# Kernel tuning notes

Hardware: AMD Instinct MI355X
Metric: run time of the kernel (lower is better)

The kernel has to match this reference:

```python
import jax, jax.numpy as jnp
import numpy as np
import math

B, T, HID = 2, 2048, 2048
NH, KVH, HD = 16, 4, 128  # num_heads, kv_heads, head_dim


def rotate_half(x):
    x1, x2 = x[..., : x.shape[-1] // 2], x[..., x.shape[-1] // 2 :]
    return jnp.concatenate([-x2, x1], axis=-1)


def setup_inputs() -> dict:
    key = jax.random.key(0)
    ks = jax.random.split(key, 6)
    hidden_states = jax.random.normal(ks[0], (B, T, HID), dtype=jnp.float32)
    # additive causal mask (0 on/below diag, -inf-ish above)
    causal = jnp.triu(jnp.full((T, T), -1e9, dtype=jnp.float32), k=1)
    attention_mask = causal[None, None, :, :]
    # real RoPE angles
    inv_freq = 1.0 / (10000.0 ** (np.arange(0, HD, 2, dtype=np.float32) / HD))
    t = np.arange(T, dtype=np.float32)
    freqs = np.einsum('t,d->td', t, inv_freq)
    emb = np.concatenate([freqs, freqs], axis=-1)  # (T, HD)
    cos = jnp.asarray(np.cos(emb))[None, None, :, :]
    sin = jnp.asarray(np.sin(emb))[None, None, :, :]
    s = 0.02
    Wq = jax.random.normal(ks[1], (HID, NH * HD), dtype=jnp.float32) * s
    Wk = jax.random.normal(ks[2], (HID, KVH * HD), dtype=jnp.float32) * s
    Wv = jax.random.normal(ks[3], (HID, KVH * HD), dtype=jnp.float32) * s
    Wo = jax.random.normal(ks[4], (HID, HID), dtype=jnp.float32) * s
    return dict(hidden_states=hidden_states, attention_mask=attention_mask,
                cos=cos, sin=sin, Wq=Wq, Wk=Wk, Wv=Wv, Wo=Wo)


def reference(hidden_states, attention_mask, cos, sin, Wq, Wk, Wv, Wo):
    b, t, _ = hidden_states.shape
    # projections; weights stored (in, out) so y = x @ W
    q = (hidden_states @ Wq).reshape(b, t, NH, HD).transpose(0, 2, 1, 3)   # (B,H,T,D)
    k = (hidden_states @ Wk).reshape(b, t, KVH, HD).transpose(0, 2, 1, 3)  # (B,Hkv,T,D)
    v = (hidden_states @ Wv).reshape(b, t, KVH, HD).transpose(0, 2, 1, 3)
    # RoPE
    c, s = cos[:, :, :t, :], sin[:, :, :t, :]
    q = q * c + rotate_half(q) * s
    k = k * c + rotate_half(k) * s
    # GQA: repeat_interleave kv heads
    rf = NH // KVH
    k = jnp.repeat(k, rf, axis=1)
    v = jnp.repeat(v, rf, axis=1)
    scores = jnp.einsum('bhtd,bhsd->bhts', q, k) / math.sqrt(HD)
    scores = scores + attention_mask
    probs = jax.nn.softmax(scores.astype(jnp.float32), axis=-1).astype(q.dtype)
    ctx = jnp.einsum('bhts,bhsd->bhtd', probs, v)
    ctx = ctx.transpose(0, 2, 1, 3).reshape(b, t, HID)
    return ctx @ Wo
```

## Files before the change

kernel.cpp:

```cpp
#include <hip/hip_runtime.h>
#include <hip/hip_bf16.h>
#include <math.h>

typedef __bf16 bf16;
typedef __bf16 bf16x4 __attribute__((ext_vector_type(4)));
typedef __bf16 bf16x8 __attribute__((ext_vector_type(8)));
typedef float f32x4 __attribute__((ext_vector_type(4)));

#define B_   2
#define T_   2048
#define HID_ 2048
#define NH_  16
#define KVH_ 4
#define HD_  128

__device__ __forceinline__ void gload_lds16(const bf16* g, bf16* l) {
    __builtin_amdgcn_global_load_lds(
        (const __attribute__((address_space(1))) unsigned int*)g,
        (__attribute__((address_space(3))) unsigned int*)l, 16, 0, 0);
}

__device__ __forceinline__ bf16x8 cat4(bf16x4 a, bf16x4 b) {
    bf16x8 r;
    #pragma unroll
    for (int i = 0; i < 4; i++) { r[i] = a[i]; r[i + 4] = b[i]; }
    return r;
}

__global__ void cast_to_bf16(const float* __restrict__ in, bf16* __restrict__ out, int n4) {
    int i = blockIdx.x * 256 + threadIdx.x;
    if (i < n4) {
        float4 v = ((const float4*)in)[i];
        bf16x4 o = { (bf16)v.x, (bf16)v.y, (bf16)v.z, (bf16)v.w };
        ((bf16x4*)out)[i] = o;
    }
}

__global__ void transpose_cast(const float* __restrict__ in, bf16* __restrict__ out,
                               int N, int rowOff, int outStride) {
    __shared__ float tile[32][33];
    int k0 = blockIdx.x * 32, n0 = blockIdx.y * 32;
    int tx = threadIdx.x & 31, ty = threadIdx.x >> 5;
    for (int i = ty; i < 32; i += 8)
        tile[i][tx] = in[(size_t)(k0 + i) * N + n0 + tx];
    __syncthreads();
    for (int i = ty; i < 32; i += 8)
        out[(size_t)(rowOff + n0 + i) * outStride + (k0 + tx)] = (bf16)tile[tx][i];
}

__global__ __launch_bounds__(256, 2) void gemm_bf16_nt(
    const bf16* __restrict__ A, const bf16* __restrict__ BT, float* __restrict__ C,
    int M, int N, int K) {
    __shared__ __align__(16) bf16 As[128 * 32];
    __shared__ __align__(16) bf16 Bs[128 * 32];
    int bm = blockIdx.x * 128, bn = blockIdx.y * 128;
    int tid = threadIdx.x, lane = tid & 63, w = tid >> 6;
    int wm = (w & 1) * 64, wn = (w >> 1) * 64;
    int lm = lane & 15, quad = lane >> 4;
    int c0 = w * 64 + lane, c1 = 256 + c0;
    int r0 = c0 >> 2, g0 = ((c0 & 3) ^ (r0 & 3)) * 8;
    int r1 = c1 >> 2, g1 = ((c1 & 3) ^ (r1 & 3)) * 8;
    const bf16* a0 = A  + (size_t)(bm + r0) * K + g0;
    const bf16* a1 = A  + (size_t)(bm + r1) * K + g1;
    const bf16* b0 = BT + (size_t)(bn + r0) * K + g0;
    const bf16* b1 = BT + (size_t)(bn + r1) * K + g1;
    bf16* lA0 = As + (size_t)(w * 64) * 8;
    bf16* lA1 = As + (size_t)(256 + w * 64) * 8;
    bf16* lB0 = Bs + (size_t)(w * 64) * 8;
    bf16* lB1 = Bs + (size_t)(256 + w * 64) * 8;
    int sx = ((quad ^ (lm & 3)) << 3);
    f32x4 acc[4][4] = {};
    for (int k0 = 0; k0 < K; k0 += 32) {
        gload_lds16(a0, lA0); gload_lds16(a1, lA1);
        gload_lds16(b0, lB0); gload_lds16(b1, lB1);
        a0 += 32; a1 += 32; b0 += 32; b1 += 32;
        __syncthreads();
        bf16x8 af[4], bfr[4];
        #pragma unroll
        for (int mt = 0; mt < 4; mt++) af[mt]  = *(const bf16x8*)&As[(wm + mt*16 + lm) * 32 + sx];
        #pragma unroll
        for (int nt = 0; nt < 4; nt++) bfr[nt] = *(const bf16x8*)&Bs[(wn + nt*16 + lm) * 32 + sx];
        #pragma unroll
        for (int mt = 0; mt < 4; mt++)
            #pragma unroll
            for (int nt = 0; nt < 4; nt++)
                acc[mt][nt] = __builtin_amdgcn_mfma_f32_16x16x32_bf16(af[mt], bfr[nt], acc[mt][nt], 0, 0, 0);
        __syncthreads();
    }
    #pragma unroll
    for (int mt = 0; mt < 4; mt++) {
        #pragma unroll
        for (int r = 0; r < 4; r++) {
            int row = bm + wm + mt*16 + quad*4 + r;
            float* cp = C + (size_t)row * N + bn + wn + lm;
            #pragma unroll
            for (int nt = 0; nt < 4; nt++)
                cp[nt*16] = acc[mt][nt][r];
        }
    }
}

__global__ void rope_scatter(const float* __restrict__ qkv,
                             const float* __restrict__ cosb, const float* __restrict__ sinb,
                             bf16* __restrict__ q, bf16* __restrict__ k, bf16* __restrict__ vT) {
    int bt = blockIdx.x;
    int b = bt >> 11, t = bt & 2047;
    const float* row = qkv + (size_t)bt * 3072;
    for (int col = threadIdx.x; col < 3072; col += 256) {
        float v = row[col];
        if (col < 2048) {
            int h = col >> 7, d = col & 127;
            float c = cosb[t*128 + d], s = sinb[t*128 + d];
            float rot = (d < 64) ? -row[col + 64] : row[col - 64];
            float val = (v * c + rot * s) * 0.12752965013239224f;
            q[((size_t)(b*NH_ + h) * T_ + t) * HD_ + d] = (bf16)val;
        } else if (col < 2560) {
            int idx = col - 2048, h = idx >> 7, d = idx & 127;
            float c = cosb[t*128 + d], s = sinb[t*128 + d];
            float rot = (d < 64) ? -row[col + 64] : row[col - 64];
            k[((size_t)(b*KVH_ + h) * T_ + t) * HD_ + d] = (bf16)(v * c + rot * s);
        } else {
            int idx = col - 2560, h = idx >> 7, d = idx & 127;
            vT[((size_t)(b*KVH_ + h) * HD_ + d) * T_ + t] = (bf16)v;
        }
    }
}

__global__ __launch_bounds__(256, 2) void flash_attn(
    const bf16* __restrict__ q, const bf16* __restrict__ k, const bf16* __restrict__ vT,
    bf16* __restrict__ ctx) {
    __shared__ __align__(16) bf16 Ks[64][136];
    __shared__ __align__(16) bf16 Vt[128][72];
    int bh = blockIdx.y;
    int b = bh >> 4, h = bh & 15, kvh = h >> 2;
    int tid = threadIdx.x, lane = tid & 63, w = tid >> 6;
    int lm = lane & 15, quad = lane >> 4, kq = quad * 8;
    const bf16* kg = k  + (size_t)(b * KVH_ + kvh) * T_ * HD_;
    const bf16* vg = vT + (size_t)(b * KVH_ + kvh) * HD_ * T_;
    int krow = tid >> 2, kcol = (tid & 3) * 32;
    int vrow = tid >> 1, vcol = (tid & 1) * 32;

    for (int half = 0; half < 2; half++) {
        int qt = (half == 0) ? blockIdx.x : (31 - blockIdx.x);
        const bf16* qg = q + ((size_t)(b * NH_ + h) * T_ + qt*64 + w*16 + lm) * HD_;
        bf16x8 qf[4];
        #pragma unroll
        for (int kk = 0; kk < 4; kk++) qf[kk] = *(const bf16x8*)(qg + kk*32 + kq);

        f32x4 Ot[8] = {};
        float l_ = 0.f;
        int nIter = qt + 1;

        bf16x8 pk[4], pv[4];
        {
            const bf16* ksrc = kg + (size_t)krow * HD_ + kcol;
            const bf16* vsrc = vg + (size_t)vrow * T_ + vcol;
            #pragma unroll
            for (int j = 0; j < 4; j++) { pk[j] = *(const bf16x8*)(ksrc + j*8); pv[j] = *(const bf16x8*)(vsrc + j*8); }
        }

        for (int it = 0; it < nIter; it++) {
            __syncthreads();
            #pragma unroll
            for (int j = 0; j < 4; j++) {
                *(bf16x8*)&Ks[krow][kcol + j*8] = pk[j];
                *(bf16x8*)&Vt[vrow][vcol + j*8] = pv[j];
            }
            __syncthreads();
            if (it + 1 < nIter) {
                int s0n = (it + 1) * 64;
                const bf16* ksrc = kg + (size_t)(s0n + krow) * HD_ + kcol;
                const bf16* vsrc = vg + (size_t)vrow * T_ + s0n + vcol;
                #pragma unroll
                for (int j = 0; j < 4; j++) { pk[j] = *(const bf16x8*)(ksrc + j*8); pv[j] = *(const bf16x8*)(vsrc + j*8); }
            }

            f32x4 sacc[4] = {};
            #pragma unroll
            for (int n = 0; n < 4; n++)
                #pragma unroll
                for (int kk = 0; kk < 4; kk++) {
                    bf16x8 kf = *(const bf16x8*)&Ks[n*16 + lm][kk*32 + kq];
                    sacc[n] = __builtin_amdgcn_mfma_f32_16x16x32_bf16(kf, qf[kk], sacc[n], 0, 0, 0);
                }
            if (it == qt) {
                #pragma unroll
                for (int n = 0; n < 4; n++)
                    #pragma unroll
                    for (int r = 0; r < 4; r++)
                        if (n*16 + quad*4 + r > w*16 + lm) sacc[n][r] = -1e30f;
            }
            bf16x4 pt[4];
            #pragma unroll
            for (int n = 0; n < 4; n++) {
                f32x4 pe;
                #pragma unroll
                for (int r = 0; r < 4; r++) pe[r] = exp2f(sacc[n][r]);
                l_ += (pe[0] + pe[1]) + (pe[2] + pe[3]);
                #pragma unroll
                for (int r = 0; r < 4; r++) pt[n][r] = (bf16)pe[r];
            }
            bf16x8 pf01 = cat4(pt[0], pt[1]);
            bf16x8 pf23 = cat4(pt[2], pt[3]);
            #pragma unroll
            for (int dt = 0; dt < 8; dt++) {
                const bf16* vr = &Vt[dt*16 + lm][0];
                bf16x8 vf01 = cat4(*(const bf16x4*)(vr + 4*quad),      *(const bf16x4*)(vr + 16 + 4*quad));
                Ot[dt] = __builtin_amdgcn_mfma_f32_16x16x32_bf16(vf01, pf01, Ot[dt], 0, 0, 0);
                bf16x8 vf23 = cat4(*(const bf16x4*)(vr + 32 + 4*quad), *(const bf16x4*)(vr + 48 + 4*quad));
                Ot[dt] = __builtin_amdgcn_mfma_f32_16x16x32_bf16(vf23, pf23, Ot[dt], 0, 0, 0);
            }
        }

        l_ += __shfl_xor(l_, 16);
        l_ += __shfl_xor(l_, 32);
        float linv = 1.0f / l_;
        bf16* cp = ctx + ((size_t)(b * T_) + qt*64 + w*16 + lm) * HID_ + h * HD_;
        #pragma unroll
        for (int dt = 0; dt < 8; dt++) {
            bf16x4 o4 = { (bf16)(Ot[dt][0]*linv), (bf16)(Ot[dt][1]*linv),
                          (bf16)(Ot[dt][2]*linv), (bf16)(Ot[dt][3]*linv) };
            *(bf16x4*)(cp + dt*16 + quad*4) = o4;
        }
    }
}

extern "C" void kernel_launch(void* const* d_in, const int* in_sizes, int n_in,
                              void* d_out, int out_size, void* d_ws, size_t ws_size,
                              hipStream_t stream) {
    const float* hidden = (const float*)d_in[0];
    const float* cosb = (const float*)d_in[2];
    const float* sinb = (const float*)d_in[3];
    const float* Wq = (const float*)d_in[4];
    const float* Wk = (const float*)d_in[5];
    const float* Wv = (const float*)d_in[6];
    const float* Wo = (const float*)d_in[7];
    float* out = (float*)d_out;

    char* ws = (char*)d_ws;
    size_t off = 0;
    bf16* hid_bf = (bf16*)(ws + off); off += (size_t)4096*2048*2;
    bf16* WqkvT  = (bf16*)(ws + off); off += (size_t)3072*2048*2;
    bf16* WoT    = (bf16*)(ws + off); off += (size_t)2048*2048*2;
    float* QKV   = (float*)(ws + off); off += (size_t)4096*3072*4;
    bf16* qbuf   = (bf16*)(ws + off); off += (size_t)B_*NH_*T_*HD_*2;
    bf16* kbuf   = (bf16*)(ws + off); off += (size_t)B_*KVH_*T_*HD_*2;
    bf16* vtbuf  = (bf16*)(ws + off); off += (size_t)B_*KVH_*HD_*T_*2;
    bf16* ctx    = (bf16*)(ws + off); off += (size_t)4096*2048*2;

    cast_to_bf16<<<8192, 256, 0, stream>>>(hidden, hid_bf, 4096*2048/4);
    transpose_cast<<<dim3(64, 64), 256, 0, stream>>>(Wq, WqkvT, 2048, 0,    2048);
    transpose_cast<<<dim3(64, 16), 256, 0, stream>>>(Wk, WqkvT, 512,  2048, 2048);
    transpose_cast<<<dim3(64, 16), 256, 0, stream>>>(Wv, WqkvT, 512,  2560, 2048);
    transpose_cast<<<dim3(64, 64), 256, 0, stream>>>(Wo, WoT,   2048, 0,    2048);

    gemm_bf16_nt<<<dim3(32, 24), 256, 0, stream>>>(hid_bf, WqkvT, QKV, 4096, 3072, 2048);
    rope_scatter<<<4096, 256, 0, stream>>>(QKV, cosb, sinb, qbuf, kbuf, vtbuf);
    flash_attn<<<dim3(16, 32), 256, 0, stream>>>(qbuf, kbuf, vtbuf, ctx);
    gemm_bf16_nt<<<dim3(32, 16), 256, 0, stream>>>(ctx, WoT, out, 4096, 2048, 2048);
}
```

Measured before the change: 350.1 us.

## Fuse RoPE and head scatter into QKV GEMM; async LDS loads in attention

```diff
diff --git a/kernel.cpp b/kernel.cpp
--- a/kernel.cpp
+++ b/kernel.cpp
@@ -46,6 +46,104 @@
     __syncthreads();
     for (int i = ty; i < 32; i += 8)
         out[(size_t)(rowOff + n0 + i) * outStride + (k0 + tx)] = (bf16)tile[tx][i];
+}
+
+
+__global__ __launch_bounds__(256, 2) void gemm_qkv_rope(
+    const bf16* __restrict__ A, const bf16* __restrict__ BT,
+    const float* __restrict__ cosb, const float* __restrict__ sinb,
+    bf16* __restrict__ q, bf16* __restrict__ k, bf16* __restrict__ vT) {
+    __shared__ __align__(16) char smem[128 * 136 * 2];
+    bf16* As = (bf16*)smem;
+    bf16* Bs = As + 128 * 32;
+    bf16* Cs = (bf16*)smem;
+    const int K = 2048;
+    int bm = blockIdx.x * 128, hid = blockIdx.y, bn = hid * 128;
+    int tid = threadIdx.x, lane = tid & 63, w = tid >> 6;
+    int wm = (w & 1) * 64, wn = (w >> 1) * 64;
+    int lm = lane & 15, quad = lane >> 4;
+    int c0 = w * 64 + lane, c1 = 256 + c0;
+    int r0 = c0 >> 2, g0 = ((c0 & 3) ^ (r0 & 3)) * 8;
+    int r1 = c1 >> 2, g1 = ((c1 & 3) ^ (r1 & 3)) * 8;
+    const bf16* a0 = A  + (size_t)(bm + r0) * K + g0;
+    const bf16* a1 = A  + (size_t)(bm + r1) * K + g1;
+    const bf16* b0 = BT + (size_t)(bn + r0) * K + g0;
+    const bf16* b1 = BT + (size_t)(bn + r1) * K + g1;
+    bf16* lA0 = As + (size_t)(w * 64) * 8;
+    bf16* lA1 = As + (size_t)(256 + w * 64) * 8;
+    bf16* lB0 = Bs + (size_t)(w * 64) * 8;
+    bf16* lB1 = Bs + (size_t)(256 + w * 64) * 8;
+    int sx = ((quad ^ (lm & 3)) << 3);
+    f32x4 acc[4][4] = {};
+    for (int k0 = 0; k0 < K; k0 += 32) {
+        gload_lds16(a0, lA0); gload_lds16(a1, lA1);
+        gload_lds16(b0, lB0); gload_lds16(b1, lB1);
+        a0 += 32; a1 += 32; b0 += 32; b1 += 32;
+        __syncthreads();
+        bf16x8 af[4], bfr[4];
+        #pragma unroll
+        for (int mt = 0; mt < 4; mt++) af[mt]  = *(const bf16x8*)&As[(wm + mt*16 + lm) * 32 + sx];
+        #pragma unroll
+        for (int nt = 0; nt < 4; nt++) bfr[nt] = *(const bf16x8*)&Bs[(wn + nt*16 + lm) * 32 + sx];
+        #pragma unroll
+        for (int mt = 0; mt < 4; mt++)
+            #pragma unroll
+            for (int nt = 0; nt < 4; nt++)
+                acc[mt][nt] = __builtin_amdgcn_mfma_f32_16x16x32_bf16(af[mt], bfr[nt], acc[mt][nt], 0, 0, 0);
+        __syncthreads();
+    }
+    #pragma unroll
+    for (int mt = 0; mt < 4; mt++)
+        #pragma unroll
+        for (int r = 0; r < 4; r++) {
+            int row = wm + mt*16 + quad*4 + r;
+            #pragma unroll
+            for (int nt = 0; nt < 4; nt++)
+                Cs[row * 136 + wn + nt*16 + lm] = (bf16)acc[mt][nt][r];
+        }
+    __syncthreads();
+
+    int b = bm >> 11, t0 = bm & 2047;
+    if (hid < 20) {
+        bool isq = hid < 16;
+        int d = (tid & 15) * 8;
+        float sgn = (d < 64) ? -1.f : 1.f;
+        float scl = isq ? 0.12752965013239224f : 1.0f;
+        bf16* dst = isq ? (q + ((size_t)(b * NH_ + hid) * T_) * HD_)
+                        : (k + ((size_t)(b * KVH_ + (hid - 16)) * T_) * HD_);
+        #pragma unroll
+        for (int i = 0; i < 8; i++) {
+            int row = (tid >> 4) + i * 16;
+            int t = t0 + row;
+            bf16x8 x  = *(const bf16x8*)&Cs[row * 136 + d];
+            bf16x8 xo = *(const bf16x8*)&Cs[row * 136 + (d ^ 64)];
+            bf16x8 o;
+            #pragma unroll
+            for (int j = 0; j < 8; j++) {
+                float c = cosb[t * 128 + d + j], s = sinb[t * 128 + d + j];
+                o[j] = (bf16)(((float)x[j] * c + sgn * (float)xo[j] * s) * scl);
+            }
+            *(bf16x8*)(dst + (size_t)t * HD_ + d) = o;
+        }
+    } else {
+        int kvh = hid - 20;
+        int t6 = (tid & 15) * 4;
+        int C = 4 * (t6 >> 5) + ((t6 >> 2) & 3);
+        int j0 = 4 * ((t6 >> 4) & 1);
+        int pos = 8 * C + j0;
+        bf16* dst = vT + (size_t)(b * KVH_ + kvh) * HD_ * T_;
+        #pragma unroll
+        for (int i = 0; i < 8; i++) {
+            int d = (tid >> 4) + i * 16;
+            #pragma unroll
+            for (int half = 0; half < 2; half++) {
+                int tt = half * 64 + t6;
+                bf16x4 vv = { Cs[(tt+0)*136 + d], Cs[(tt+1)*136 + d],
+                              Cs[(tt+2)*136 + d], Cs[(tt+3)*136 + d] };
+                *(bf16x4*)(dst + (size_t)d * T_ + t0 + half * 64 + pos) = vv;
+            }
+        }
+    }
 }
 
 __global__ __launch_bounds__(256, 2) void gemm_bf16_nt(
@@ -100,45 +198,25 @@
     }
 }
 
-__global__ void rope_scatter(const float* __restrict__ qkv,
-                             const float* __restrict__ cosb, const float* __restrict__ sinb,
-                             bf16* __restrict__ q, bf16* __restrict__ k, bf16* __restrict__ vT) {
-    int bt = blockIdx.x;
-    int b = bt >> 11, t = bt & 2047;
-    const float* row = qkv + (size_t)bt * 3072;
-    for (int col = threadIdx.x; col < 3072; col += 256) {
-        float v = row[col];
-        if (col < 2048) {
-            int h = col >> 7, d = col & 127;
-            float c = cosb[t*128 + d], s = sinb[t*128 + d];
-            float rot = (d < 64) ? -row[col + 64] : row[col - 64];
-            float val = (v * c + rot * s) * 0.12752965013239224f;
-            q[((size_t)(b*NH_ + h) * T_ + t) * HD_ + d] = (bf16)val;
-        } else if (col < 2560) {
-            int idx = col - 2048, h = idx >> 7, d = idx & 127;
-            float c = cosb[t*128 + d], s = sinb[t*128 + d];
-            float rot = (d < 64) ? -row[col + 64] : row[col - 64];
-            k[((size_t)(b*KVH_ + h) * T_ + t) * HD_ + d] = (bf16)(v * c + rot * s);
-        } else {
-            int idx = col - 2560, h = idx >> 7, d = idx & 127;
-            vT[((size_t)(b*KVH_ + h) * HD_ + d) * T_ + t] = (bf16)v;
-        }
-    }
-}
-
 __global__ __launch_bounds__(256, 2) void flash_attn(
     const bf16* __restrict__ q, const bf16* __restrict__ k, const bf16* __restrict__ vT,
     bf16* __restrict__ ctx) {
-    __shared__ __align__(16) bf16 Ks[64][136];
-    __shared__ __align__(16) bf16 Vt[128][72];
+    __shared__ __align__(16) bf16 Ks[64 * 128];
+    __shared__ __align__(16) bf16 Vp[128 * 64];
     int bh = blockIdx.y;
     int b = bh >> 4, h = bh & 15, kvh = h >> 2;
     int tid = threadIdx.x, lane = tid & 63, w = tid >> 6;
     int lm = lane & 15, quad = lane >> 4, kq = quad * 8;
     const bf16* kg = k  + (size_t)(b * KVH_ + kvh) * T_ * HD_;
     const bf16* vg = vT + (size_t)(b * KVH_ + kvh) * HD_ * T_;
-    int krow = tid >> 2, kcol = (tid & 3) * 32;
-    int vrow = tid >> 1, vcol = (tid & 1) * 32;
+    int ksl = lane >> 4;
+    int kko = ((lane >> 2) & 3) * 32;
+    int kc  = ((lane & 3) ^ ((lane >> 4) & 3)) * 8;
+    int vdl = lane >> 3;
+    int vc  = ((lane & 7) ^ ((lane >> 3) & 7)) * 8;
+    int sxk = (quad ^ (lm & 3)) << 3;
+    int sxv1 = ((quad ^ (lm & 7)) << 3);
+    int sxv2 = (((4 + quad) ^ (lm & 7)) << 3);
 
     for (int half = 0; half < 2; half++) {
         int qt = (half == 0) ? blockIdx.x : (31 - blockIdx.x);
@@ -151,36 +229,26 @@
         float l_ = 0.f;
         int nIter = qt + 1;
 
-        bf16x8 pk[4], pv[4];
-        {
-            const bf16* ksrc = kg + (size_t)krow * HD_ + kcol;
-            const bf16* vsrc = vg + (size_t)vrow * T_ + vcol;
-            #pragma unroll
-            for (int j = 0; j < 4; j++) { pk[j] = *(const bf16x8*)(ksrc + j*8); pv[j] = *(const bf16x8*)(vsrc + j*8); }
-        }
-
         for (int it = 0; it < nIter; it++) {
+            int s0 = it * 64;
+            #pragma unroll
+            for (int i = 0; i < 4; i++) {
+                int srow = w * 16 + i * 4;
+                gload_lds16(kg + (size_t)(s0 + srow + ksl) * HD_ + kko + kc, Ks + srow * 128);
+            }
+            #pragma unroll
+            for (int i = 0; i < 4; i++) {
+                int drow = w * 32 + i * 8;
+                gload_lds16(vg + (size_t)(drow + vdl) * T_ + s0 + vc, Vp + drow * 64);
+            }
             __syncthreads();
-            #pragma unroll
-            for (int j = 0; j < 4; j++) {
-                *(bf16x8*)&Ks[krow][kcol + j*8] = pk[j];
-                *(bf16x8*)&Vt[vrow][vcol + j*8] = pv[j];
-            }
-            __syncthreads();
-            if (it + 1 < nIter) {
-                int s0n = (it + 1) * 64;
-                const bf16* ksrc = kg + (size_t)(s0n + krow) * HD_ + kcol;
-                const bf16* vsrc = vg + (size_t)vrow * T_ + s0n + vcol;
-                #pragma unroll
-                for (int j = 0; j < 4; j++) { pk[j] = *(const bf16x8*)(ksrc + j*8); pv[j] = *(const bf16x8*)(vsrc + j*8); }
-            }
 
             f32x4 sacc[4] = {};
             #pragma unroll
             for (int n = 0; n < 4; n++)
                 #pragma unroll
                 for (int kk = 0; kk < 4; kk++) {
-                    bf16x8 kf = *(const bf16x8*)&Ks[n*16 + lm][kk*32 + kq];
+                    bf16x8 kf = *(const bf16x8*)&Ks[(n*16 + lm) * 128 + kk*32 + sxk];
                     sacc[n] = __builtin_amdgcn_mfma_f32_16x16x32_bf16(kf, qf[kk], sacc[n], 0, 0, 0);
                 }
             if (it == qt) {
@@ -204,12 +272,13 @@
             bf16x8 pf23 = cat4(pt[2], pt[3]);
             #pragma unroll
             for (int dt = 0; dt < 8; dt++) {
-                const bf16* vr = &Vt[dt*16 + lm][0];
-                bf16x8 vf01 = cat4(*(const bf16x4*)(vr + 4*quad),      *(const bf16x4*)(vr + 16 + 4*quad));
+                const bf16* vr = &Vp[(dt*16 + lm) * 64];
+                bf16x8 vf01 = *(const bf16x8*)(vr + sxv1);
                 Ot[dt] = __builtin_amdgcn_mfma_f32_16x16x32_bf16(vf01, pf01, Ot[dt], 0, 0, 0);
-                bf16x8 vf23 = cat4(*(const bf16x4*)(vr + 32 + 4*quad), *(const bf16x4*)(vr + 48 + 4*quad));
+                bf16x8 vf23 = *(const bf16x8*)(vr + sxv2);
                 Ot[dt] = __builtin_amdgcn_mfma_f32_16x16x32_bf16(vf23, pf23, Ot[dt], 0, 0, 0);
             }
+            __syncthreads();
         }
 
         l_ += __shfl_xor(l_, 16);
@@ -242,7 +311,6 @@
     bf16* hid_bf = (bf16*)(ws + off); off += (size_t)4096*2048*2;
     bf16* WqkvT  = (bf16*)(ws + off); off += (size_t)3072*2048*2;
     bf16* WoT    = (bf16*)(ws + off); off += (size_t)2048*2048*2;
-    float* QKV   = (float*)(ws + off); off += (size_t)4096*3072*4;
     bf16* qbuf   = (bf16*)(ws + off); off += (size_t)B_*NH_*T_*HD_*2;
     bf16* kbuf   = (bf16*)(ws + off); off += (size_t)B_*KVH_*T_*HD_*2;
     bf16* vtbuf  = (bf16*)(ws + off); off += (size_t)B_*KVH_*HD_*T_*2;
@@ -254,8 +322,7 @@
     transpose_cast<<<dim3(64, 16), 256, 0, stream>>>(Wv, WqkvT, 512,  2560, 2048);
     transpose_cast<<<dim3(64, 64), 256, 0, stream>>>(Wo, WoT,   2048, 0,    2048);
 
-    gemm_bf16_nt<<<dim3(32, 24), 256, 0, stream>>>(hid_bf, WqkvT, QKV, 4096, 3072, 2048);
-    rope_scatter<<<4096, 256, 0, stream>>>(QKV, cosb, sinb, qbuf, kbuf, vtbuf);
+    gemm_qkv_rope<<<dim3(32, 24), 256, 0, stream>>>(hid_bf, WqkvT, cosb, sinb, qbuf, kbuf, vtbuf);
     flash_attn<<<dim3(16, 32), 256, 0, stream>>>(qbuf, kbuf, vtbuf, ctx);
     gemm_bf16_nt<<<dim3(32, 16), 256, 0, stream>>>(ctx, WoT, out, 4096, 2048, 2048);
 }
```

Measured after the change: 330.0 us. -5.8%, faster.
